# Performance work log

Measured on AMD Instinct MI355X. Metric: run time of the kernel, lower is better.

## Reference

```python
import jax, jax.numpy as jnp
import numpy as np

HID = 1024   # hidden_size
HEADS = 16   # multi_head
DH = 64      # hidden_size_head
FF = 4096    # ff_size
EPS = 1e-6   # LayerNorm epsilon
NEG = -1e9


def setup_inputs() -> dict:
    key = jax.random.key(0)
    ks = jax.random.split(key, 24)
    B, LI, LQ, LK = 16, 512, 64, 128
    s = 0.02

    def w(k, shape):
        return jax.random.normal(k, shape, jnp.float32) * s

    return {
        "img_feat": jax.random.normal(ks[0], (B, LI, HID), jnp.float32),
        "ques": jax.random.normal(ks[1], (B, LQ, HID), jnp.float32),
        "kg": jax.random.normal(ks[2], (B, LK, HID), jnp.float32),
        "ques_mask": jax.random.randint(ks[3], (B, LQ), 0, 2, jnp.int32),
        "kg_mask": jax.random.randint(ks[4], (B, LK), 0, 2, jnp.int32),
        # stacked params for the 3 MHAtt blocks; torch Linear weight layout [out, in]
        "att_qw": w(ks[5], (3, HID, HID)), "att_qb": jnp.zeros((3, HID), jnp.float32),
        "att_kw": w(ks[6], (3, HID, HID)), "att_kb": jnp.zeros((3, HID), jnp.float32),
        "att_vw": w(ks[7], (3, HID, HID)), "att_vb": jnp.zeros((3, HID), jnp.float32),
        "att_ow": w(ks[8], (3, HID, HID)), "att_ob": jnp.zeros((3, HID), jnp.float32),
        "ffn_w1": w(ks[9], (FF, HID)), "ffn_b1": jnp.zeros((FF,), jnp.float32),
        "ffn_w2": w(ks[10], (HID, FF)), "ffn_b2": jnp.zeros((HID,), jnp.float32),
        "ln_g": jnp.ones((4, HID), jnp.float32), "ln_b": jnp.zeros((4, HID), jnp.float32),
    }


def _ln(x, g, b):
    m = jnp.mean(x, axis=-1, keepdims=True)
    v = jnp.mean(jnp.square(x - m), axis=-1, keepdims=True)
    return g * (x - m) / jnp.sqrt(v + EPS) + b


def _mha(v_in, k_in, q_in, mask, qw, qb, kw, kb, vw, vb, ow, ob):
    B = q_in.shape[0]

    def proj(x, wt, bi):  # [B,S,H] -> [B,heads,S,DH]
        y = jnp.einsum('bsh,oh->bso', x, wt) + bi
        return y.reshape(B, -1, HEADS, DH).transpose(0, 2, 1, 3)

    q = proj(q_in, qw, qb)
    k = proj(k_in, kw, kb)
    v = proj(v_in, vw, vb)
    scores = jnp.einsum('bhqd,bhkd->bhqk', q, k) / jnp.sqrt(jnp.float32(DH))
    if mask is not None:
        scores = jnp.where(mask[:, None, None, :] == 1, NEG, scores)
    a = jax.nn.softmax(scores, axis=-1)  # dropout is identity at eval
    o = jnp.einsum('bhqk,bhkd->bhqd', a, v).transpose(0, 2, 1, 3).reshape(B, -1, HID)
    return jnp.einsum('bsh,oh->bso', o, ow) + ob


def reference(img_feat, ques, kg, ques_mask, kg_mask,
              att_qw, att_qb, att_kw, att_kb, att_vw, att_vb, att_ow, att_ob,
              ffn_w1, ffn_b1, ffn_w2, ffn_b2, ln_g, ln_b):
    x = img_feat
    # self-attention on image features (no mask)
    x = _ln(x + _mha(x, x, x, None,
                     att_qw[0], att_qb[0], att_kw[0], att_kb[0],
                     att_vw[0], att_vb[0], att_ow[0], att_ob[0]), ln_g[0], ln_b[0])
    # cross-attention to question
    x = _ln(x + _mha(ques, ques, x, ques_mask,
                     att_qw[1], att_qb[1], att_kw[1], att_kb[1],
                     att_vw[1], att_vb[1], att_ow[1], att_ob[1]), ln_g[1], ln_b[1])
    # cross-attention to knowledge graph facts
    x = _ln(x + _mha(kg, kg, x, kg_mask,
                     att_qw[2], att_qb[2], att_kw[2], att_kb[2],
                     att_vw[2], att_vb[2], att_ow[2], att_ob[2]), ln_g[2], ln_b[2])
    # FFN: Linear -> ReLU -> Linear (dropout identity at eval)
    h = jax.nn.relu(jnp.einsum('bsh,fh->bsf', x, ffn_w1) + ffn_b1)
    f = jnp.einsum('bsf,hf->bsh', h, ffn_w2) + ffn_b2
    x = _ln(x + f, ln_g[3], ln_b[3])
    return x
```

## Files before the change

### kernel.cpp

```cpp
#include <hip/hip_runtime.h>
#include <math.h>

#define HIDN 1024
#define NHEADS 16
#define DHEAD 64
#define FFD 4096
#define LN_EPS 1e-6f
#define NEGV -1e9f

typedef __bf16 bf16_t;
typedef __bf16 bf16x8 __attribute__((ext_vector_type(8)));
typedef float f32x4 __attribute__((ext_vector_type(4)));
typedef unsigned short ushort8 __attribute__((ext_vector_type(8)));
typedef unsigned short ushort4v __attribute__((ext_vector_type(4)));

__device__ __forceinline__ unsigned short f2bf(float f) {
    unsigned u = __float_as_uint(f);
    return (unsigned short)((u + 0x7FFFu + ((u >> 16) & 1u)) >> 16);
}
__device__ __forceinline__ float bf2f(unsigned short u) {
    return __uint_as_float((unsigned)u << 16);
}
__device__ __forceinline__ void gld16(const void* g, void* l) {
    __builtin_amdgcn_global_load_lds(
        (const __attribute__((address_space(1))) void*)g,
        (__attribute__((address_space(3))) void*)l, 16, 0, 0);
}

template<int RELU>
__global__ __launch_bounds__(256)
void gemm_mfma(const bf16_t* __restrict__ A, const bf16_t* __restrict__ W,
               const float* __restrict__ ba, const float* __restrict__ bb,
               const float* __restrict__ bc, const float* __restrict__ bd,
               unsigned short* __restrict__ Cb, int M, int N, int K)
{
    __shared__ __align__(16) bf16_t As[2][128 * 64];
    __shared__ __align__(16) bf16_t Bs[2][128 * 64];

    const int tid  = threadIdx.x;
    const int wid  = tid >> 6;
    const int lane = tid & 63;
    const int m0 = blockIdx.x * 128;
    const int n0 = blockIdx.y * 128;
    const int wm = (wid & 1) * 64;
    const int wn = (wid >> 1) * 64;

    const int sr = (wid << 3) + (lane >> 3);
    const int sk = (((lane & 7) ^ (lane >> 3)) * 8);
    const bf16_t* pa = A + (size_t)(m0 + sr) * K + sk;
    const bf16_t* pb = W + (size_t)(n0 + sr) * K + sk;
    const int lofs = (wid << 3) * 64;

    const int lr  = lane & 15;
    const int hi_ = lane >> 4;
    const int ch0 = ((hi_ + 0) ^ (lane & 7)) * 8;
    const int ch1 = ((hi_ + 4) ^ (lane & 7)) * 8;

    f32x4 acc[4][4];
    #pragma unroll
    for (int i = 0; i < 4; ++i)
        #pragma unroll
        for (int j = 0; j < 4; ++j) acc[i][j] = (f32x4){0.f, 0.f, 0.f, 0.f};

    auto stage = [&](int buf, int koff) {
        #pragma unroll
        for (int c = 0; c < 4; ++c) {
            gld16(pa + (size_t)c * 32 * K + koff, &As[buf][lofs + c * 32 * 64]);
            gld16(pb + (size_t)c * 32 * K + koff, &Bs[buf][lofs + c * 32 * 64]);
        }
    };
    auto compute = [&](int buf) {
        const bf16_t* fa = &As[buf][(wm + lr) * 64];
        const bf16_t* fb = &Bs[buf][(wn + lr) * 64];
        #pragma unroll
        for (int kk = 0; kk < 2; ++kk) {
            const int ch = kk ? ch1 : ch0;
            bf16x8 a[4], b[4];
            #pragma unroll
            for (int i = 0; i < 4; ++i) {
                a[i] = *(const bf16x8*)(fa + i * 16 * 64 + ch);
                b[i] = *(const bf16x8*)(fb + i * 16 * 64 + ch);
            }
            #pragma unroll
            for (int i = 0; i < 4; ++i)
                #pragma unroll
                for (int j = 0; j < 4; ++j)
                    acc[i][j] = __builtin_amdgcn_mfma_f32_16x16x32_bf16(
                        a[i], b[j], acc[i][j], 0, 0, 0);
        }
    };

    stage(0, 0);
    asm volatile("s_waitcnt vmcnt(0)" ::: "memory");
    __syncthreads();

    for (int k0 = 0; k0 < K; k0 += 128) {
        if (k0 + 64 < K) stage(1, k0 + 64);
        compute(0);
        asm volatile("s_waitcnt vmcnt(0)" ::: "memory");
        __syncthreads();
        if (k0 + 128 < K) stage(0, k0 + 128);
        compute(1);
        asm volatile("s_waitcnt vmcnt(0)" ::: "memory");
        __syncthreads();
    }

    const int seg = n0 >> 10;
    const float* bias = (seg == 0) ? ba : (seg == 1) ? bb : (seg == 2) ? bc : bd;
    const int nl = (n0 & 1023);
    const int er = wm + (lane >> 4) * 4;
    const int ec = wn + (lane & 15);
    float bv[4];
    #pragma unroll
    for (int j = 0; j < 4; ++j) bv[j] = bias[nl + ec + j * 16];
    #pragma unroll
    for (int i = 0; i < 4; ++i)
        #pragma unroll
        for (int j = 0; j < 4; ++j)
            #pragma unroll
            for (int r = 0; r < 4; ++r) {
                float v = acc[i][j][r] + bv[j];
                if (RELU) v = fmaxf(v, 0.f);
                Cb[(size_t)(m0 + er + i * 16 + r) * N + (n0 + ec + j * 16)] = f2bf(v);
            }
}

template<int HAS_MASK>
__global__ __launch_bounds__(256)
void attn_mfma(const bf16_t* __restrict__ Q, const bf16_t* __restrict__ K,
               const bf16_t* __restrict__ V, int qstride, int kvstride,
               const int* __restrict__ mask,
               unsigned short* __restrict__ O, int Lk)
{
    __shared__ __align__(16) unsigned short Ks[64][72];
    __shared__ __align__(16) unsigned short Vt[64][72];
    __shared__ __align__(16) unsigned short Ps[64][72];
    __shared__ int smask[64];

    const int tid  = threadIdx.x;
    const int wid  = tid >> 6;
    const int lane = tid & 63;
    const int lo   = lane & 15;
    const int hi   = lane >> 4;
    const int q0   = blockIdx.x * 64;
    const int h    = blockIdx.y;
    const int b    = blockIdx.z;
    const int Lq   = 512;

    bf16x8 qf[2];
    {
        const bf16_t* qp = Q + (size_t)(b*Lq + q0 + wid*16 + lo) * qstride + h*DHEAD + hi*8;
        qf[0] = *(const bf16x8*)qp;
        qf[1] = *(const bf16x8*)(qp + 32);
    }

    float mrun[4], lrun[4];
    f32x4 Oc[4];
    #pragma unroll
    for (int r = 0; r < 4; ++r) { mrun[r] = -INFINITY; lrun[r] = 0.f; }
    #pragma unroll
    for (int n = 0; n < 4; ++n) Oc[n] = (f32x4){0.f, 0.f, 0.f, 0.f};

    const int sr = tid >> 2;
    const int sc = (tid & 3) * 16;

    for (int k0 = 0; k0 < Lk; k0 += 64) {
        {
            const bf16_t* kp = K + (size_t)(b*Lk + k0 + sr) * kvstride + h*DHEAD + sc;
            *(bf16x8*)&Ks[sr][sc]     = *(const bf16x8*)kp;
            *(bf16x8*)&Ks[sr][sc + 8] = *(const bf16x8*)(kp + 8);
            const unsigned short* vp = (const unsigned short*)
                (V + (size_t)(b*Lk + k0 + sr) * kvstride + h*DHEAD + sc);
            ushort8 v0 = *(const ushort8*)vp;
            ushort8 v1 = *(const ushort8*)(vp + 8);
            #pragma unroll
            for (int t = 0; t < 8; ++t) {
                Vt[sc + t][sr]     = v0[t];
                Vt[sc + 8 + t][sr] = v1[t];
            }
            if (HAS_MASK && tid < 64) smask[tid] = mask[b*Lk + k0 + tid];
        }
        __syncthreads();

        f32x4 s[4];
        #pragma unroll
        for (int j = 0; j < 4; ++j) s[j] = (f32x4){0.f, 0.f, 0.f, 0.f};
        #pragma unroll
        for (int kk = 0; kk < 2; ++kk) {
            #pragma unroll
            for (int j = 0; j < 4; ++j) {
                bf16x8 bfrag = *(const bf16x8*)&Ks[j*16 + lo][kk*32 + hi*8];
                s[j] = __builtin_amdgcn_mfma_f32_16x16x32_bf16(qf[kk], bfrag, s[j], 0, 0, 0);
            }
        }
        #pragma unroll
        for (int j = 0; j < 4; ++j) {
            bool msk = HAS_MASK ? (smask[j*16 + lo] != 0) : false;
            #pragma unroll
            for (int r = 0; r < 4; ++r) {
                float sv = s[j][r] * 0.125f;
                s[j][r] = msk ? NEGV : sv;
            }
        }

        #pragma unroll
        for (int r = 0; r < 4; ++r) {
            float tm = fmaxf(fmaxf(s[0][r], s[1][r]), fmaxf(s[2][r], s[3][r]));
            #pragma unroll
            for (int m = 1; m < 16; m <<= 1) tm = fmaxf(tm, __shfl_xor(tm, m));
            float mnew = fmaxf(mrun[r], tm);
            float f = __expf(mrun[r] - mnew);
            float ps = 0.f;
            #pragma unroll
            for (int j = 0; j < 4; ++j) {
                float p = __expf(s[j][r] - mnew);
                s[j][r] = p;
                ps += p;
            }
            #pragma unroll
            for (int m = 1; m < 16; m <<= 1) ps += __shfl_xor(ps, m);
            lrun[r] = lrun[r] * f + ps;
            mrun[r] = mnew;
            #pragma unroll
            for (int n = 0; n < 4; ++n) Oc[n][r] *= f;
            #pragma unroll
            for (int j = 0; j < 4; ++j)
                Ps[wid*16 + hi*4 + r][j*16 + lo] = f2bf(s[j][r]);
        }

        #pragma unroll
        for (int kk = 0; kk < 2; ++kk) {
            bf16x8 pa = *(const bf16x8*)&Ps[wid*16 + lo][kk*32 + hi*8];
            #pragma unroll
            for (int n = 0; n < 4; ++n) {
                bf16x8 vf = *(const bf16x8*)&Vt[n*16 + lo][kk*32 + hi*8];
                Oc[n] = __builtin_amdgcn_mfma_f32_16x16x32_bf16(pa, vf, Oc[n], 0, 0, 0);
            }
        }
        __syncthreads();
    }

    #pragma unroll
    for (int r = 0; r < 4; ++r) {
        float inv = 1.f / lrun[r];
        const size_t row = (size_t)(b*Lq + q0 + wid*16 + hi*4 + r) * HIDN + h*DHEAD;
        #pragma unroll
        for (int n = 0; n < 4; ++n)
            O[row + n*16 + lo] = f2bf(Oc[n][r] * inv);
    }
}

template<int WF32, int WBF>
__global__ __launch_bounds__(256)
void ln_res_b(const unsigned short* __restrict__ X, const unsigned short* __restrict__ R,
              const float* __restrict__ G, const float* __restrict__ Bv,
              unsigned short* __restrict__ OutB, float* __restrict__ OutF)
{
    const int row = blockIdx.x;
    const int tid = threadIdx.x;
    const size_t base = (size_t)row * HIDN + tid * 4;
    ushort4v xv = *(const ushort4v*)(X + base);
    ushort4v rv = *(const ushort4v*)(R + base);
    float y[4];
    #pragma unroll
    for (int t = 0; t < 4; ++t) y[t] = bf2f(xv[t]) + bf2f(rv[t]);
    float s1 = y[0] + y[1] + y[2] + y[3];
    float s2 = y[0]*y[0] + y[1]*y[1] + y[2]*y[2] + y[3]*y[3];
    #pragma unroll
    for (int m = 1; m < 64; m <<= 1) {
        s1 += __shfl_xor(s1, m);
        s2 += __shfl_xor(s2, m);
    }
    __shared__ float red1[4], red2[4];
    const int wave = tid >> 6, lane = tid & 63;
    if (lane == 0) { red1[wave] = s1; red2[wave] = s2; }
    __syncthreads();
    s1 = red1[0] + red1[1] + red1[2] + red1[3];
    s2 = red2[0] + red2[1] + red2[2] + red2[3];
    const float mean = s1 * (1.f / HIDN);
    const float var  = s2 * (1.f / HIDN) - mean * mean;
    const float inv  = rsqrtf(var + LN_EPS);
    float4 gv = *(const float4*)(G + tid*4);
    float4 bv = *(const float4*)(Bv + tid*4);
    float o[4];
    o[0] = gv.x * (y[0]-mean) * inv + bv.x;
    o[1] = gv.y * (y[1]-mean) * inv + bv.y;
    o[2] = gv.z * (y[2]-mean) * inv + bv.z;
    o[3] = gv.w * (y[3]-mean) * inv + bv.w;
    if (WBF) {
        ushort4v ob;
        #pragma unroll
        for (int t = 0; t < 4; ++t) ob[t] = f2bf(o[t]);
        *(ushort4v*)(OutB + base) = ob;
    }
    if (WF32) {
        float4 of = {o[0], o[1], o[2], o[3]};
        *(float4*)(OutF + base) = of;
    }
}

struct CvtArgs {
    const float* src[32];
    unsigned short* dst[32];
};

__global__ __launch_bounds__(256)
void cvt_units(CvtArgs args)
{
    const float* s = args.src[blockIdx.y];
    unsigned short* d = args.dst[blockIdx.y];
    const int i = blockIdx.x * 256 + threadIdx.x;
    const float4* p = (const float4*)s + (size_t)i * 2;
    float4 a = p[0], b = p[1];
    ushort8 o;
    o[0] = f2bf(a.x); o[1] = f2bf(a.y); o[2] = f2bf(a.z); o[3] = f2bf(a.w);
    o[4] = f2bf(b.x); o[5] = f2bf(b.y); o[6] = f2bf(b.z); o[7] = f2bf(b.w);
    ((ushort8*)d)[i] = o;
}

extern "C" void kernel_launch(void* const* d_in, const int* in_sizes, int n_in,
                              void* d_out, int out_size, void* d_ws, size_t ws_size,
                              hipStream_t stream)
{
    const float* img   = (const float*)d_in[0];
    const float* ques  = (const float*)d_in[1];
    const float* kg    = (const float*)d_in[2];
    const int*   qmask = (const int*)d_in[3];
    const int*   kmask = (const int*)d_in[4];
    const float* qw = (const float*)d_in[5];
    const float* qb = (const float*)d_in[6];
    const float* kw = (const float*)d_in[7];
    const float* kb = (const float*)d_in[8];
    const float* vw = (const float*)d_in[9];
    const float* vb = (const float*)d_in[10];
    const float* ow = (const float*)d_in[11];
    const float* ob = (const float*)d_in[12];
    const float* w1 = (const float*)d_in[13];
    const float* b1 = (const float*)d_in[14];
    const float* w2 = (const float*)d_in[15];
    const float* b2 = (const float*)d_in[16];
    const float* lng = (const float*)d_in[17];
    const float* lnb = (const float*)d_in[18];
    float* out = (float*)d_out;

    const int B = 16;
    const int NX = B * 512;
    const size_t WSTEP = (size_t)1024 * 1024;
    const size_t MB = (size_t)1 << 20;
    const size_t MELEM = (size_t)1024 * 1024;

    char* wsb = (char*)d_ws;
    unsigned short* xb    = (unsigned short*)(wsb);
    unsigned short* bM    = (unsigned short*)(wsb + 16*MB);
    unsigned short* bOb   = (unsigned short*)(wsb + 32*MB);
    unsigned short* quesb = (unsigned short*)(wsb + 48*MB);
    unsigned short* kgb   = (unsigned short*)(wsb + 50*MB);
    unsigned short* wa    = (unsigned short*)(wsb + 56*MB);
    unsigned short* bQKV  = (unsigned short*)(wsb + 96*MB);
    unsigned short* bKV   = (unsigned short*)(wsb + 144*MB);
    unsigned short* hb    = (unsigned short*)(wsb + 96*MB);

    CvtArgs ca;
    int u = 0;
    auto addu = [&](const float* src, int melems, unsigned short* dst) {
        for (int i = 0; i < melems; ++i) {
            ca.src[u] = src + (size_t)i * MELEM;
            ca.dst[u] = dst + (size_t)i * MELEM;
            ++u;
        }
    };
    addu(qw + 0*WSTEP, 1, wa + 0*MELEM);
    addu(kw + 0*WSTEP, 1, wa + 1*MELEM);
    addu(vw + 0*WSTEP, 1, wa + 2*MELEM);
    addu(qw + 1*WSTEP, 1, wa + 3*MELEM);
    addu(kw + 1*WSTEP, 1, wa + 4*MELEM);
    addu(vw + 1*WSTEP, 1, wa + 5*MELEM);
    addu(qw + 2*WSTEP, 1, wa + 6*MELEM);
    addu(kw + 2*WSTEP, 1, wa + 7*MELEM);
    addu(vw + 2*WSTEP, 1, wa + 8*MELEM);
    addu(ow + 0*WSTEP, 1, wa + 9*MELEM);
    addu(ow + 1*WSTEP, 1, wa + 10*MELEM);
    addu(ow + 2*WSTEP, 1, wa + 11*MELEM);
    addu(w1, 4, wa + 12*MELEM);
    addu(w2, 4, wa + 16*MELEM);
    addu(img,  8, xb);
    addu(ques, 1, quesb);
    addu(kg,   2, kgb);

    dim3 blk(256);
    cvt_units<<<dim3(512, u), blk, 0, stream>>>(ca);

    auto gemm = [&](const unsigned short* A, const unsigned short* W,
                    const float* ba, const float* bb_, const float* bc, const float* bd,
                    unsigned short* C, int M, int N, int K, int relu) {
        dim3 grid(M / 128, N / 128);
        if (relu) gemm_mfma<1><<<grid, blk, 0, stream>>>(
            (const bf16_t*)A, (const bf16_t*)W, ba, bb_, bc, bd, C, M, N, K);
        else      gemm_mfma<0><<<grid, blk, 0, stream>>>(
            (const bf16_t*)A, (const bf16_t*)W, ba, bb_, bc, bd, C, M, N, K);
    };

    const unsigned short* Akv[3] = {xb, quesb, kgb};
    const int Mkv[3] = {NX, B * 64, B * 128};
    const int Lk[3]  = {512, 64, 128};

    for (int t = 0; t < 3; ++t) {
        if (t == 0) {
            gemm(xb, wa + 0*MELEM, qb + 0, kb + 0, vb + 0, vb + 0,
                 bQKV, NX, 3072, 1024, 0);
            attn_mfma<0><<<dim3(8, NHEADS, B), blk, 0, stream>>>(
                (const bf16_t*)bQKV, (const bf16_t*)bQKV + 1024, (const bf16_t*)bQKV + 2048,
                3072, 3072, nullptr, bOb, Lk[t]);
        } else {
            gemm(xb, wa + (t == 1 ? 3 : 6)*MELEM,
                 qb + t*1024, qb + t*1024, qb + t*1024, qb + t*1024,
                 bQKV, NX, 1024, 1024, 0);
            gemm(Akv[t], wa + (t == 1 ? 4 : 7)*MELEM,
                 kb + t*1024, vb + t*1024, vb + t*1024, vb + t*1024,
                 bKV, Mkv[t], 2048, 1024, 0);
            attn_mfma<1><<<dim3(8, NHEADS, B), blk, 0, stream>>>(
                (const bf16_t*)bQKV, (const bf16_t*)bKV, (const bf16_t*)bKV + 1024,
                1024, 2048, (t == 1 ? qmask : kmask), bOb, Lk[t]);
        }
        gemm(bOb, wa + (9 + t)*MELEM,
             ob + t*1024, ob + t*1024, ob + t*1024, ob + t*1024,
             bM, NX, 1024, 1024, 0);
        ln_res_b<0,1><<<NX, blk, 0, stream>>>(xb, bM, lng + t*1024, lnb + t*1024, xb, nullptr);
    }

    gemm(xb, wa + 12*MELEM, b1, b1 + 1024, b1 + 2048, b1 + 3072, hb, NX, FFD, 1024, 1);
    gemm(hb, wa + 16*MELEM, b2, b2, b2, b2, bM, NX, 1024, 4096, 0);
    ln_res_b<1,0><<<NX, blk, 0, stream>>>(xb, bM, lng + 3*1024, lnb + 3*1024, nullptr, out);
}
```

Measured before the change: 517.9 us.

## Restructure attention to one block per head with K/V reuse and prefetch

The attention kernel now launches one 512-thread block per (head, batch) that handles all 512 query rows, so each K/V tile is loaded once and reused across four query sub-tiles instead of being reloaded by eight separate blocks. The next K/V tile is prefetched into registers while the current one is computed, K and V loads are split across thread halves, and XOR swizzles are applied to the K and transposed V shared-memory tiles to cut bank conflicts. The grid shrinks to 256 blocks, which risks under-filling the GPU, and the larger per-thread state (four sets of accumulators and Q fragments) raises register pressure.

```diff
diff --git a/kernel.cpp b/kernel.cpp
--- a/kernel.cpp
+++ b/kernel.cpp
@@ -126,7 +126,7 @@
 }
 
 template<int HAS_MASK>
-__global__ __launch_bounds__(256)
+__global__ __launch_bounds__(512, 2)
 void attn_mfma(const bf16_t* __restrict__ Q, const bf16_t* __restrict__ K,
                const bf16_t* __restrict__ V, int qstride, int kvstride,
                const int* __restrict__ mask,
@@ -134,7 +134,7 @@
 {
     __shared__ __align__(16) unsigned short Ks[64][72];
     __shared__ __align__(16) unsigned short Vt[64][72];
-    __shared__ __align__(16) unsigned short Ps[64][72];
+    __shared__ __align__(16) unsigned short Ps[128][72];
     __shared__ int smask[64];
 
     const int tid  = threadIdx.x;
@@ -142,112 +142,156 @@
     const int lane = tid & 63;
     const int lo   = lane & 15;
     const int hi   = lane >> 4;
-    const int q0   = blockIdx.x * 64;
-    const int h    = blockIdx.y;
-    const int b    = blockIdx.z;
+    const int h    = blockIdx.x;
+    const int b    = blockIdx.y;
     const int Lq   = 512;
 
-    bf16x8 qf[2];
-    {
-        const bf16_t* qp = Q + (size_t)(b*Lq + q0 + wid*16 + lo) * qstride + h*DHEAD + hi*8;
-        qf[0] = *(const bf16x8*)qp;
-        qf[1] = *(const bf16x8*)(qp + 32);
-    }
-
-    float mrun[4], lrun[4];
-    f32x4 Oc[4];
-    #pragma unroll
-    for (int r = 0; r < 4; ++r) { mrun[r] = -INFINITY; lrun[r] = 0.f; }
-    #pragma unroll
-    for (int n = 0; n < 4; ++n) Oc[n] = (f32x4){0.f, 0.f, 0.f, 0.f};
-
-    const int sr = tid >> 2;
-    const int sc = (tid & 3) * 16;
-
-    for (int k0 = 0; k0 < Lk; k0 += 64) {
-        {
-            const bf16_t* kp = K + (size_t)(b*Lk + k0 + sr) * kvstride + h*DHEAD + sc;
-            *(bf16x8*)&Ks[sr][sc]     = *(const bf16x8*)kp;
-            *(bf16x8*)&Ks[sr][sc + 8] = *(const bf16x8*)(kp + 8);
+    bf16x8 qf[4][2];
+    #pragma unroll
+    for (int s4 = 0; s4 < 4; ++s4) {
+        const bf16_t* qp = Q + (size_t)(b*Lq + s4*128 + wid*16 + lo) * qstride
+                             + h*DHEAD + hi*8;
+        qf[s4][0] = *(const bf16x8*)qp;
+        qf[s4][1] = *(const bf16x8*)(qp + 32);
+    }
+
+    float mrun[4][4], lrun[4][4];
+    f32x4 Oc[4][4];
+    #pragma unroll
+    for (int s4 = 0; s4 < 4; ++s4)
+        #pragma unroll
+        for (int r = 0; r < 4; ++r) {
+            mrun[s4][r] = -INFINITY; lrun[s4][r] = 0.f;
+            Oc[s4][r] = (f32x4){0.f, 0.f, 0.f, 0.f};
+        }
+
+    ushort8 r0, r1;
+    int mreg = 0;
+
+    auto load_tile = [&](int k0) {
+        if (tid < 256) {
+            const int sr = tid >> 2, sc = (tid & 3) * 16;
+            const unsigned short* kp = (const unsigned short*)
+                (K + (size_t)(b*Lk + k0 + sr) * kvstride + h*DHEAD + sc);
+            r0 = *(const ushort8*)kp;
+            r1 = *(const ushort8*)(kp + 8);
+        } else {
+            const int t2 = tid - 256, sr = t2 >> 2, sc = (t2 & 3) * 16;
             const unsigned short* vp = (const unsigned short*)
                 (V + (size_t)(b*Lk + k0 + sr) * kvstride + h*DHEAD + sc);
-            ushort8 v0 = *(const ushort8*)vp;
-            ushort8 v1 = *(const ushort8*)(vp + 8);
+            r0 = *(const ushort8*)vp;
+            r1 = *(const ushort8*)(vp + 8);
+        }
+        if (HAS_MASK && tid < 64) mreg = mask[b*Lk + k0 + tid];
+    };
+    auto store_tile = [&]() {
+        if (tid < 256) {
+            const int sr = tid >> 2, sc = (tid & 3) * 16;
+            const int x = ((sr >> 3) & 7) << 3;
+            *(ushort8*)&Ks[sr][sc ^ x]       = r0;
+            *(ushort8*)&Ks[sr][(sc + 8) ^ x] = r1;
+        } else {
+            const int t2 = tid - 256, sr = t2 >> 2, sc = (t2 & 3) * 16;
             #pragma unroll
             for (int t = 0; t < 8; ++t) {
-                Vt[sc + t][sr]     = v0[t];
-                Vt[sc + 8 + t][sr] = v1[t];
-            }
-            if (HAS_MASK && tid < 64) smask[tid] = mask[b*Lk + k0 + tid];
-        }
+                const int d0 = sc + t, d1 = sc + 8 + t;
+                Vt[d0][sr ^ (((d0 >> 3) & 7) << 3)] = r0[t];
+                Vt[d1][sr ^ (((d1 >> 3) & 7) << 3)] = r1[t];
+            }
+        }
+        if (HAS_MASK && tid < 64) smask[tid] = mreg;
+    };
+
+    load_tile(0);
+    store_tile();
+    __syncthreads();
+
+    int k0 = 0;
+    while (true) {
+        const bool more = (k0 + 64 < Lk);
+        if (more) load_tile(k0 + 64);
+
+        #pragma unroll
+        for (int s4 = 0; s4 < 4; ++s4) {
+            f32x4 sv[4];
+            #pragma unroll
+            for (int j = 0; j < 4; ++j) sv[j] = (f32x4){0.f, 0.f, 0.f, 0.f};
+            #pragma unroll
+            for (int kk = 0; kk < 2; ++kk) {
+                #pragma unroll
+                for (int j = 0; j < 4; ++j) {
+                    const int krow = j*16 + lo;
+                    const int kcol = (kk*32 + hi*8) ^ (((krow >> 3) & 7) << 3);
+                    bf16x8 bfrag = *(const bf16x8*)&Ks[krow][kcol];
+                    sv[j] = __builtin_amdgcn_mfma_f32_16x16x32_bf16(
+                        qf[s4][kk], bfrag, sv[j], 0, 0, 0);
+                }
+            }
+            #pragma unroll
+            for (int j = 0; j < 4; ++j) {
+                bool msk = HAS_MASK ? (smask[j*16 + lo] != 0) : false;
+                #pragma unroll
+                for (int r = 0; r < 4; ++r) {
+                    float x = sv[j][r] * 0.125f;
+                    sv[j][r] = msk ? NEGV : x;
+                }
+            }
+            #pragma unroll
+            for (int r = 0; r < 4; ++r) {
+                float tm = fmaxf(fmaxf(sv[0][r], sv[1][r]), fmaxf(sv[2][r], sv[3][r]));
+                #pragma unroll
+                for (int m = 1; m < 16; m <<= 1) tm = fmaxf(tm, __shfl_xor(tm, m));
+                float mnew = fmaxf(mrun[s4][r], tm);
+                float f = __expf(mrun[s4][r] - mnew);
+                float ps = 0.f;
+                #pragma unroll
+                for (int j = 0; j < 4; ++j) {
+                    float p = __expf(sv[j][r] - mnew);
+                    sv[j][r] = p;
+                    ps += p;
+                }
+                #pragma unroll
+                for (int m = 1; m < 16; m <<= 1) ps += __shfl_xor(ps, m);
+                lrun[s4][r] = lrun[s4][r] * f + ps;
+                mrun[s4][r] = mnew;
+                #pragma unroll
+                for (int n = 0; n < 4; ++n) Oc[s4][n][r] *= f;
+                #pragma unroll
+                for (int j = 0; j < 4; ++j)
+                    Ps[wid*16 + hi*4 + r][j*16 + lo] = f2bf(sv[j][r]);
+            }
+            #pragma unroll
+            for (int kk = 0; kk < 2; ++kk) {
+                bf16x8 pa = *(const bf16x8*)&Ps[wid*16 + lo][kk*32 + hi*8];
+                #pragma unroll
+                for (int n = 0; n < 4; ++n) {
+                    const int vrow = n*16 + lo;
+                    const int vcol = (kk*32 + hi*8) ^ (((vrow >> 3) & 7) << 3);
+                    bf16x8 vf = *(const bf16x8*)&Vt[vrow][vcol];
+                    Oc[s4][n] = __builtin_amdgcn_mfma_f32_16x16x32_bf16(
+                        pa, vf, Oc[s4][n], 0, 0, 0);
+                }
+            }
+        }
+
+        if (!more) break;
         __syncthreads();
-
-        f32x4 s[4];
-        #pragma unroll
-        for (int j = 0; j < 4; ++j) s[j] = (f32x4){0.f, 0.f, 0.f, 0.f};
-        #pragma unroll
-        for (int kk = 0; kk < 2; ++kk) {
-            #pragma unroll
-            for (int j = 0; j < 4; ++j) {
-                bf16x8 bfrag = *(const bf16x8*)&Ks[j*16 + lo][kk*32 + hi*8];
-                s[j] = __builtin_amdgcn_mfma_f32_16x16x32_bf16(qf[kk], bfrag, s[j], 0, 0, 0);
-            }
-        }
-        #pragma unroll
-        for (int j = 0; j < 4; ++j) {
-            bool msk = HAS_MASK ? (smask[j*16 + lo] != 0) : false;
-            #pragma unroll
-            for (int r = 0; r < 4; ++r) {
-                float sv = s[j][r] * 0.125f;
-                s[j][r] = msk ? NEGV : sv;
-            }
-        }
-
+        store_tile();
+        __syncthreads();
+        k0 += 64;
+    }
+
+    #pragma unroll
+    for (int s4 = 0; s4 < 4; ++s4)
         #pragma unroll
         for (int r = 0; r < 4; ++r) {
-            float tm = fmaxf(fmaxf(s[0][r], s[1][r]), fmaxf(s[2][r], s[3][r]));
-            #pragma unroll
-            for (int m = 1; m < 16; m <<= 1) tm = fmaxf(tm, __shfl_xor(tm, m));
-            float mnew = fmaxf(mrun[r], tm);
-            float f = __expf(mrun[r] - mnew);
-            float ps = 0.f;
-            #pragma unroll
-            for (int j = 0; j < 4; ++j) {
-                float p = __expf(s[j][r] - mnew);
-                s[j][r] = p;
-                ps += p;
-            }
-            #pragma unroll
-            for (int m = 1; m < 16; m <<= 1) ps += __shfl_xor(ps, m);
-            lrun[r] = lrun[r] * f + ps;
-            mrun[r] = mnew;
-            #pragma unroll
-            for (int n = 0; n < 4; ++n) Oc[n][r] *= f;
-            #pragma unroll
-            for (int j = 0; j < 4; ++j)
-                Ps[wid*16 + hi*4 + r][j*16 + lo] = f2bf(s[j][r]);
-        }
-
-        #pragma unroll
-        for (int kk = 0; kk < 2; ++kk) {
-            bf16x8 pa = *(const bf16x8*)&Ps[wid*16 + lo][kk*32 + hi*8];
-            #pragma unroll
-            for (int n = 0; n < 4; ++n) {
-                bf16x8 vf = *(const bf16x8*)&Vt[n*16 + lo][kk*32 + hi*8];
-                Oc[n] = __builtin_amdgcn_mfma_f32_16x16x32_bf16(pa, vf, Oc[n], 0, 0, 0);
-            }
-        }
-        __syncthreads();
-    }
-
-    #pragma unroll
-    for (int r = 0; r < 4; ++r) {
-        float inv = 1.f / lrun[r];
-        const size_t row = (size_t)(b*Lq + q0 + wid*16 + hi*4 + r) * HIDN + h*DHEAD;
-        #pragma unroll
-        for (int n = 0; n < 4; ++n)
-            O[row + n*16 + lo] = f2bf(Oc[n][r] * inv);
-    }
+            float inv = 1.f / lrun[s4][r];
+            const size_t row = (size_t)(b*Lq + s4*128 + wid*16 + hi*4 + r) * HIDN
+                             + h*DHEAD;
+            #pragma unroll
+            for (int n = 0; n < 4; ++n)
+                O[row + n*16 + lo] = f2bf(Oc[s4][n][r] * inv);
+        }
 }
 
 template<int WF32, int WBF>
@@ -404,11 +448,14 @@
     const int Mkv[3] = {NX, B * 64, B * 128};
     const int Lk[3]  = {512, 64, 128};
 
+    dim3 ablk(512);
+    dim3 agrid(NHEADS, B);
+
     for (int t = 0; t < 3; ++t) {
         if (t == 0) {
             gemm(xb, wa + 0*MELEM, qb + 0, kb + 0, vb + 0, vb + 0,
                  bQKV, NX, 3072, 1024, 0);
-            attn_mfma<0><<<dim3(8, NHEADS, B), blk, 0, stream>>>(
+            attn_mfma<0><<<agrid, ablk, 0, stream>>>(
                 (const bf16_t*)bQKV, (const bf16_t*)bQKV + 1024, (const bf16_t*)bQKV + 2048,
                 3072, 3072, nullptr, bOb, Lk[t]);
         } else {
@@ -418,7 +465,7 @@
             gemm(Akv[t], wa + (t == 1 ? 4 : 7)*MELEM,
                  kb + t*1024, vb + t*1024, vb + t*1024, vb + t*1024,
                  bKV, Mkv[t], 2048, 1024, 0);
-            attn_mfma<1><<<dim3(8, NHEADS, B), blk, 0, stream>>>(
+            attn_mfma<1><<<agrid, ablk, 0, stream>>>(
                 (const bf16_t*)bQKV, (const bf16_t*)bKV, (const bf16_t*)bKV + 1024,
                 1024, 2048, (t == 1 ? qmask : kmask), bOb, Lk[t]);
         }
```

After: 505.6 us. -2.4%, faster.
